# Optimization experiments

Hardware: AMD Instinct MI355X
Metric: run time of the kernel (lower is better)

The kernel has to match this reference:

```python
import jax, jax.numpy as jnp
import numpy as np
import math

CHUNK = 128  # hardcoded chunk_size in the original module


def setup_inputs() -> dict:
    key = jax.random.key(0)
    ks = jax.random.split(key, 6)
    B, C, T, H, W = 8, 256, 16, 8, 8
    KC, VC = 8192, 512  # key_channels, value_channels (dk = KC/heads = T*H*W = 1024)
    return {
        "x": jax.random.normal(ks[0], (B, C, T, H, W), dtype=jnp.float32),
        "Wk": jax.random.normal(ks[1], (KC, C), dtype=jnp.float32) * 0.02,
        "Wq": jax.random.normal(ks[2], (KC, C), dtype=jnp.float32) * 0.02,
        "Wv": jax.random.normal(ks[3], (VC, C), dtype=jnp.float32) * 0.02,
        "Wr": jax.random.normal(ks[4], (C, VC), dtype=jnp.float32) * 0.02,
        "br": jnp.zeros((C,), dtype=jnp.float32),
        "num_heads": 8,
    }


def reference(x, Wk, Wq, Wv, Wr, br, num_heads):
    B, C, T, H, W = x.shape
    N = T * H * W
    # 1x1x1 Conv3d == per-position linear projection
    k = jnp.einsum('oc,bcthw->bothw', Wk, x).reshape(B, num_heads, -1, N)
    q = jnp.einsum('oc,bcthw->bothw', Wq, x).reshape(B, num_heads, -1, N)
    v = jnp.einsum('oc,bcthw->bothw', Wv, x).reshape(B, num_heads, -1, N)
    dk = k.shape[2]  # == N by structural constraint of the original matmul
    # matmul(keys, q_chunk) over all chunks at once (matmul is linear in q):
    # contracts keys' position axis with queries' channel axis, as in torch.
    scores = jnp.matmul(k, q) / math.sqrt(dk)  # [B, h, dk, N]
    # softmax applied per query-chunk of size CHUNK along the last axis
    nchunks = N // CHUNK
    attn = jax.nn.softmax(
        scores.reshape(B, num_heads, dk, nchunks, CHUNK), axis=-1
    ).reshape(B, num_heads, dk, N)
    out = jnp.matmul(v, attn)  # [B, h, dv, N] (dk == N)
    out = out.reshape(B, -1, T, H, W)
    out = jnp.einsum('oc,bcthw->bothw', Wr, out) + br[None, :, None, None, None]
    return out
```

## Files before the change

kernel.cpp:

```cpp
#include <hip/hip_runtime.h>
#include <hip/hip_bf16.h>


using bf16x8 = __attribute__((ext_vector_type(8))) __bf16;
using f32x4  = __attribute__((ext_vector_type(4))) float;
using s16x4  = __attribute__((ext_vector_type(4))) short;

static __device__ __forceinline__ short f2b(float f) {
  union { float f; unsigned u; } v; v.f = f;
  unsigned r = v.u + 0x7fffu + ((v.u >> 16) & 1u);
  return (short)(r >> 16);
}

#define MFMA16(a, b, c) __builtin_amdgcn_mfma_f32_16x16x32_bf16((a), (b), (c), 0, 0, 0)

__global__ __launch_bounds__(256) void cvt_bf16(const float* __restrict__ in,
                                                short* __restrict__ out, int n) {
  int i = (blockIdx.x * 256 + threadIdx.x) * 4;
  if (i >= n) return;
  float4 v = *(const float4*)(in + i);
  s16x4 s = { f2b(v.x), f2b(v.y), f2b(v.z), f2b(v.w) };
  *(s16x4*)(out + i) = s;
}

__global__ __launch_bounds__(256) void tcvt(const float* __restrict__ in,
    short* __restrict__ outP, short* __restrict__ outT,
    int R, int C, long inB, long pB, long tB)
{
  __shared__ short tile[64][68];
  long bz = blockIdx.z;
  const float* src = in + bz * inB;
  int r0 = blockIdx.y * 64, c0 = blockIdx.x * 64;
  int t = threadIdx.x;
  int r = t >> 2, cq = (t & 3) * 16;
  #pragma unroll
  for (int e = 0; e < 16; e += 4) {
    float4 v = *(const float4*)(&src[(long)(r0 + r) * C + (c0 + cq + e)]);
    s16x4 s = { f2b(v.x), f2b(v.y), f2b(v.z), f2b(v.w) };
    *(s16x4*)(&tile[r][cq + e]) = s;
    if (outP) *(s16x4*)(&outP[bz * pB + (long)(r0 + r) * C + (c0 + cq + e)]) = s;
  }
  __syncthreads();
  int tr = t >> 2, re = (t & 3) * 16;
  short tmp[16];
  #pragma unroll
  for (int e = 0; e < 16; ++e) tmp[e] = tile[re + e][tr];
  short* dst = &outT[bz * tB + (long)(c0 + tr) * R + (r0 + re)];
  #pragma unroll
  for (int e = 0; e < 16; e += 4) *(s16x4*)(&dst[e]) = *(const s16x4*)(&tmp[e]);
}

template<bool F32OUT>
__global__ __launch_bounds__(256) void gemm_nt(
    const short* __restrict__ A, const short* __restrict__ B,
    void* __restrict__ C, const float* __restrict__ bias,
    int M, int N, int K, int lda, int ldb, int ldc,
    long aSB, long aSH, long bSB, long bSH, long cSB, long cSH, int nh)
{
  int batch = blockIdx.z;
  int hb = batch % nh, bb = batch / nh;
  const short* Ab = A + bb * aSB + hb * aSH;
  const short* Bb = B + bb * bSB + hb * bSH;
  long cOff = bb * cSB + hb * cSH;
  int m0 = blockIdx.y * 128, n0 = blockIdx.x * 128;
  __shared__ short As[128 * 72];
  __shared__ short Bs[128 * 72];
  int t = threadIdx.x;
  int lane = t & 63, wid = t >> 6;
  int wm = (wid >> 1) * 64, wn = (wid & 1) * 64;
  int rl = lane & 15, q = lane >> 4;
  f32x4 acc[4][4] = {};
  for (int k0 = 0; k0 < K; k0 += 64) {
    __syncthreads();
    #pragma unroll
    for (int it = 0; it < 4; ++it) {
      int e = (t + 256 * it) * 8;
      int row = e >> 6, col = e & 63;
      *(int4*)(&As[row * 72 + col]) = *(const int4*)(&Ab[(long)(m0 + row) * lda + (k0 + col)]);
      *(int4*)(&Bs[row * 72 + col]) = *(const int4*)(&Bb[(long)(n0 + row) * ldb + (k0 + col)]);
    }
    __syncthreads();
    #pragma unroll
    for (int kt = 0; kt < 2; ++kt) {
      int kq = kt * 32 + q * 8;
      bf16x8 af[4], bfv[4];
      #pragma unroll
      for (int mi = 0; mi < 4; ++mi) af[mi] = *(const bf16x8*)(&As[(wm + 16 * mi + rl) * 72 + kq]);
      #pragma unroll
      for (int ni = 0; ni < 4; ++ni) bfv[ni] = *(const bf16x8*)(&Bs[(wn + 16 * ni + rl) * 72 + kq]);
      #pragma unroll
      for (int mi = 0; mi < 4; ++mi)
        #pragma unroll
        for (int ni = 0; ni < 4; ++ni)
          acc[mi][ni] = MFMA16(af[mi], bfv[ni], acc[mi][ni]);
    }
  }
  #pragma unroll
  for (int mi = 0; mi < 4; ++mi)
    #pragma unroll
    for (int ni = 0; ni < 4; ++ni)
      #pragma unroll
      for (int r = 0; r < 4; ++r) {
        int row = m0 + wm + 16 * mi + 4 * q + r;
        int col = n0 + wn + 16 * ni + rl;
        float val = acc[mi][ni][r];
        if (F32OUT) {
          ((float*)C)[cOff + (long)row * ldc + col] = val + (bias ? bias[row] : 0.f);
        } else {
          ((short*)C)[cOff + (long)row * ldc + col] = f2b(val);
        }
      }
}

__global__ __launch_bounds__(256) void attn_fused(
    const short* __restrict__ Wk, const short* __restrict__ GT,
    const short* __restrict__ V, short* __restrict__ OT)
{
  __shared__ short smem[18432];
  short* As = smem;
  short* Bs = smem + 9216;
  short* aT = smem;
  int blk = blockIdx.x;
  int c = blk & 7, h = (blk >> 3) & 7, b = blk >> 6;
  int t = threadIdx.x, lane = t & 63, w = t >> 6;
  int rl = lane & 15, q = lane >> 4;
  const short* Wkh = Wk + (long)(h * 1024) * 256;
  const short* GTc = GT + ((long)(b * 8 + h) * 1024 + c * 128) * 256;
  const short* Vb  = V + (long)(b * 512 + h * 64) * 1024;
  f32x4 ot[2][4] = {};
  const float SC = 1.4426950408889634f / 32.0f;

  for (int ri = 0; ri < 8; ++ri) {
    f32x4 s[2][8] = {};
    for (int k0 = 0; k0 < 256; k0 += 64) {
      __syncthreads();
      #pragma unroll
      for (int it = 0; it < 4; ++it) {
        int e = (t + 256 * it) * 8;
        int row = e >> 6, col = e & 63;
        *(int4*)(&As[row * 72 + col]) = *(const int4*)(&Wkh[(long)(ri * 128 + row) * 256 + (k0 + col)]);
        *(int4*)(&Bs[row * 72 + col]) = *(const int4*)(&GTc[(long)row * 256 + (k0 + col)]);
      }
      __syncthreads();
      #pragma unroll
      for (int kt = 0; kt < 2; ++kt) {
        int kq = kt * 32 + q * 8;
        bf16x8 af[2], bfv[8];
        af[0] = *(const bf16x8*)(&As[(w * 32 + rl) * 72 + kq]);
        af[1] = *(const bf16x8*)(&As[(w * 32 + 16 + rl) * 72 + kq]);
        #pragma unroll
        for (int ni = 0; ni < 8; ++ni) bfv[ni] = *(const bf16x8*)(&Bs[(16 * ni + rl) * 72 + kq]);
        #pragma unroll
        for (int mi = 0; mi < 2; ++mi)
          #pragma unroll
          for (int ni = 0; ni < 8; ++ni)
            s[mi][ni] = MFMA16(af[mi], bfv[ni], s[mi][ni]);
      }
    }
    float mx[2][4], sm[2][4], rc[2][4];
    #pragma unroll
    for (int mi = 0; mi < 2; ++mi)
      #pragma unroll
      for (int r = 0; r < 4; ++r) {
        float m = s[mi][0][r];
        #pragma unroll
        for (int ni = 1; ni < 8; ++ni) m = fmaxf(m, s[mi][ni][r]);
        mx[mi][r] = m;
      }
    #pragma unroll
    for (int msk = 1; msk < 16; msk <<= 1)
      #pragma unroll
      for (int mi = 0; mi < 2; ++mi)
        #pragma unroll
        for (int r = 0; r < 4; ++r)
          mx[mi][r] = fmaxf(mx[mi][r], __shfl_xor(mx[mi][r], msk, 64));
    #pragma unroll
    for (int mi = 0; mi < 2; ++mi)
      #pragma unroll
      for (int r = 0; r < 4; ++r) sm[mi][r] = 0.f;
    #pragma unroll
    for (int mi = 0; mi < 2; ++mi)
      #pragma unroll
      for (int ni = 0; ni < 8; ++ni)
        #pragma unroll
        for (int r = 0; r < 4; ++r) {
          float p = exp2f((s[mi][ni][r] - mx[mi][r]) * SC);
          s[mi][ni][r] = p;
          sm[mi][r] += p;
        }
    #pragma unroll
    for (int msk = 1; msk < 16; msk <<= 1)
      #pragma unroll
      for (int mi = 0; mi < 2; ++mi)
        #pragma unroll
        for (int r = 0; r < 4; ++r)
          sm[mi][r] += __shfl_xor(sm[mi][r], msk, 64);
    #pragma unroll
    for (int mi = 0; mi < 2; ++mi)
      #pragma unroll
      for (int r = 0; r < 4; ++r) rc[mi][r] = __builtin_amdgcn_rcpf(sm[mi][r]);

    __syncthreads();
    #pragma unroll
    for (int mi = 0; mi < 2; ++mi)
      #pragma unroll
      for (int ni = 0; ni < 8; ++ni) {
        s16x4 pk = { f2b(s[mi][ni][0] * rc[mi][0]), f2b(s[mi][ni][1] * rc[mi][1]),
                     f2b(s[mi][ni][2] * rc[mi][2]), f2b(s[mi][ni][3] * rc[mi][3]) };
        int j  = 16 * ni + rl;
        int iL = 32 * w + 16 * mi + 4 * q;
        *(s16x4*)(&aT[j * 136 + iL]) = pk;
      }
    __syncthreads();
    #pragma unroll
    for (int kt = 0; kt < 4; ++kt) {
      int kq = kt * 32 + q * 8;
      bf16x8 pa[2], vb[4];
      pa[0] = *(const bf16x8*)(&aT[(32 * w + rl) * 136 + kq]);
      pa[1] = *(const bf16x8*)(&aT[(32 * w + 16 + rl) * 136 + kq]);
      #pragma unroll
      for (int nd = 0; nd < 4; ++nd)
        vb[nd] = *(const bf16x8*)(&Vb[(long)(16 * nd + rl) * 1024 + (ri * 128 + kq)]);
      #pragma unroll
      for (int mi = 0; mi < 2; ++mi)
        #pragma unroll
        for (int nd = 0; nd < 4; ++nd)
          ot[mi][nd] = MFMA16(pa[mi], vb[nd], ot[mi][nd]);
    }
  }
  short* OTb = OT + (long)(b * 1024 + c * 128) * 512 + h * 64;
  #pragma unroll
  for (int mi = 0; mi < 2; ++mi)
    #pragma unroll
    for (int nd = 0; nd < 4; ++nd)
      #pragma unroll
      for (int r = 0; r < 4; ++r) {
        int j = 32 * w + 16 * mi + 4 * q + r;
        int d = 16 * nd + rl;
        OTb[(long)j * 512 + d] = f2b(ot[mi][nd][r]);
      }
}

extern "C" void kernel_launch(void* const* d_in, const int* in_sizes, int n_in,
                              void* d_out, int out_size, void* d_ws, size_t ws_size,
                              hipStream_t stream)
{
  const float* x  = (const float*)d_in[0];
  const float* Wk = (const float*)d_in[1];
  const float* Wq = (const float*)d_in[2];
  const float* Wv = (const float*)d_in[3];
  const float* Wr = (const float*)d_in[4];
  const float* br = (const float*)d_in[5];
  float* out = (float*)d_out;

  char* ws = (char*)d_ws;
  short* Xbf = (short*)(ws + 0);
  short* XT  = (short*)(ws + 4194304);
  short* WqT = (short*)(ws + 8388608);
  short* Wkb = (short*)(ws + 12582912);
  short* Wvb = (short*)(ws + 16777216);
  short* Wrb = (short*)(ws + 17039360);
  short* Mb  = (short*)(ws + 17301504);
  short* GTb = (short*)(ws + 25690112);
  short* Vbf = (short*)(ws + 59244544);
  short* OTb = (short*)(ws + 67633152);

  tcvt<<<dim3(16, 4, 8), 256, 0, stream>>>(x, Xbf, XT, 256, 1024, 262144L, 262144L, 262144L);
  tcvt<<<dim3(4, 128, 1), 256, 0, stream>>>(Wq, nullptr, WqT, 8192, 256, 0L, 0L, 0L);
  cvt_bf16<<<2048, 256, 0, stream>>>(Wk, Wkb, 2097152);
  cvt_bf16<<<128, 256, 0, stream>>>(Wv, Wvb, 131072);
  cvt_bf16<<<128, 256, 0, stream>>>(Wr, Wrb, 131072);

  gemm_nt<false><<<dim3(2, 2, 64), 256, 0, stream>>>(Xbf, WqT, Mb, nullptr,
      256, 256, 1024, 1024, 8192, 256,
      262144L, 0L, 0L, 1024L, 524288L, 65536L, 8);
  gemm_nt<false><<<dim3(2, 8, 64), 256, 0, stream>>>(XT, Mb, GTb, nullptr,
      1024, 256, 256, 256, 256, 256,
      262144L, 0L, 524288L, 65536L, 2097152L, 262144L, 8);
  gemm_nt<false><<<dim3(8, 4, 8), 256, 0, stream>>>(Wvb, XT, Vbf, nullptr,
      512, 1024, 256, 256, 256, 1024,
      0L, 0L, 262144L, 0L, 524288L, 0L, 1);
  attn_fused<<<512, 256, 0, stream>>>(Wkb, GTb, Vbf, OTb);
  gemm_nt<true><<<dim3(8, 2, 8), 256, 0, stream>>>(Wrb, OTb, out, br,
      256, 1024, 512, 512, 512, 1024,
      0L, 0L, 524288L, 0L, 262144L, 0L, 1);
}
```

Baseline: 310.9 us.

## Use direct global-to-LDS loads with XOR swizzle and double-buffer Wk in attention

Replaces register-staged LDS fills in the projection GEMM and the fused attention kernel with global_load_lds 16-byte transfers into XOR-swizzled LDS tiles, removing the padding. The attention kernel now keeps the whole GT chunk resident in LDS and double-buffers the Wk tiles across 256-row groups, so each block does four larger score passes instead of eight. The P·V step is split into two halves through a swizzled transpose buffer. It uses 128KB of LDS with launch bounds of one block, which lowers occupancy and raises register pressure from the wider score accumulators.

New measurement: 291.4 us. -6.3%, faster.

```diff
diff --git a/kernel.cpp b/kernel.cpp
--- a/kernel.cpp
+++ b/kernel.cpp
@@ -10,6 +10,12 @@
   union { float f; unsigned u; } v; v.f = f;
   unsigned r = v.u + 0x7fffu + ((v.u >> 16) & 1u);
   return (short)(r >> 16);
+}
+
+static __device__ __forceinline__ void gll16(const void* g, void* l) {
+  __builtin_amdgcn_global_load_lds(
+      (const __attribute__((address_space(1))) void*)g,
+      (__attribute__((address_space(3))) void*)l, 16, 0, 0);
 }
 
 #define MFMA16(a, b, c) __builtin_amdgcn_mfma_f32_16x16x32_bf16((a), (b), (c), 0, 0, 0)
@@ -63,8 +69,8 @@
   const short* Bb = B + bb * bSB + hb * bSH;
   long cOff = bb * cSB + hb * cSH;
   int m0 = blockIdx.y * 128, n0 = blockIdx.x * 128;
-  __shared__ short As[128 * 72];
-  __shared__ short Bs[128 * 72];
+  __shared__ short As[128 * 64];
+  __shared__ short Bs[128 * 64];
   int t = threadIdx.x;
   int lane = t & 63, wid = t >> 6;
   int wm = (wid >> 1) * 64, wn = (wid & 1) * 64;
@@ -73,21 +79,28 @@
   for (int k0 = 0; k0 < K; k0 += 64) {
     __syncthreads();
     #pragma unroll
-    for (int it = 0; it < 4; ++it) {
-      int e = (t + 256 * it) * 8;
-      int row = e >> 6, col = e & 63;
-      *(int4*)(&As[row * 72 + col]) = *(const int4*)(&Ab[(long)(m0 + row) * lda + (k0 + col)]);
-      *(int4*)(&Bs[row * 72 + col]) = *(const int4*)(&Bb[(long)(n0 + row) * ldb + (k0 + col)]);
+    for (int j = 0; j < 4; ++j) {
+      int g = j * 256 + t;
+      int r = g >> 3, cc = g & 7;
+      int cs = cc ^ (r & 7);
+      gll16(&Ab[(long)(m0 + r) * lda + k0 + cs * 8], (char*)As + (j * 256 + wid * 64) * 16);
+      gll16(&Bb[(long)(n0 + r) * ldb + k0 + cs * 8], (char*)Bs + (j * 256 + wid * 64) * 16);
     }
     __syncthreads();
     #pragma unroll
     for (int kt = 0; kt < 2; ++kt) {
-      int kq = kt * 32 + q * 8;
+      int cq = kt * 4 + q;
       bf16x8 af[4], bfv[4];
       #pragma unroll
-      for (int mi = 0; mi < 4; ++mi) af[mi] = *(const bf16x8*)(&As[(wm + 16 * mi + rl) * 72 + kq]);
-      #pragma unroll
-      for (int ni = 0; ni < 4; ++ni) bfv[ni] = *(const bf16x8*)(&Bs[(wn + 16 * ni + rl) * 72 + kq]);
+      for (int mi = 0; mi < 4; ++mi) {
+        int R = wm + 16 * mi + rl;
+        af[mi] = *(const bf16x8*)((const char*)As + (R * 8 + (cq ^ (R & 7))) * 16);
+      }
+      #pragma unroll
+      for (int ni = 0; ni < 4; ++ni) {
+        int RN = wn + 16 * ni + rl;
+        bfv[ni] = *(const bf16x8*)((const char*)Bs + (RN * 8 + (cq ^ (RN & 7))) * 16);
+      }
       #pragma unroll
       for (int mi = 0; mi < 4; ++mi)
         #pragma unroll
@@ -112,14 +125,15 @@
       }
 }
 
-__global__ __launch_bounds__(256) void attn_fused(
+__global__ __launch_bounds__(256, 1) void attn_fused(
     const short* __restrict__ Wk, const short* __restrict__ GT,
     const short* __restrict__ V, short* __restrict__ OT)
 {
-  __shared__ short smem[18432];
-  short* As = smem;
-  short* Bs = smem + 9216;
-  short* aT = smem;
+  __shared__ short smem[65536];
+  short* Bs  = smem;
+  short* Ab0 = smem + 32768;
+  short* Ab1 = smem + 40960;
+  short* aT  = smem + 49152;
   int blk = blockIdx.x;
   int c = blk & 7, h = (blk >> 3) & 7, b = blk >> 6;
   int t = threadIdx.x, lane = t & 63, w = t >> 6;
@@ -130,36 +144,66 @@
   f32x4 ot[2][4] = {};
   const float SC = 1.4426950408889634f / 32.0f;
 
-  for (int ri = 0; ri < 8; ++ri) {
-    f32x4 s[2][8] = {};
-    for (int k0 = 0; k0 < 256; k0 += 64) {
+  #pragma unroll
+  for (int j = 0; j < 16; ++j) {
+    int g = j * 256 + t;
+    int r = g >> 5, cc = g & 31;
+    int cs = cc ^ (r & 7);
+    gll16(&GTc[(long)r * 256 + cs * 8], (char*)Bs + (j * 256 + w * 64) * 16);
+  }
+  {
+    #pragma unroll
+    for (int j = 0; j < 4; ++j) {
+      int g = j * 256 + t;
+      int r = g >> 2, cc = g & 3;
+      int cs = cc ^ ((r >> 1) & 3);
+      gll16(&Wkh[(long)r * 256 + cs * 8], (char*)Ab0 + (j * 256 + w * 64) * 16);
+    }
+  }
+  __syncthreads();
+
+  short* Acur = Ab0;
+  short* Anxt = Ab1;
+  for (int o = 0; o < 4; ++o) {
+    f32x4 s[4][8] = {};
+    for (int k0i = 0; k0i < 8; ++k0i) {
+      int k0 = k0i * 32;
+      int nRow = -1, nK = 0;
+      if (k0i < 7)      { nRow = o * 256;      nK = k0 + 32; }
+      else if (o < 3)   { nRow = (o + 1) * 256; nK = 0; }
+      if (nRow >= 0) {
+        #pragma unroll
+        for (int j = 0; j < 4; ++j) {
+          int g = j * 256 + t;
+          int r = g >> 2, cc = g & 3;
+          int cs = cc ^ ((r >> 1) & 3);
+          gll16(&Wkh[(long)(nRow + r) * 256 + nK + cs * 8],
+                (char*)Anxt + (j * 256 + w * 64) * 16);
+        }
+      }
+      bf16x8 af[4], bv[8];
+      #pragma unroll
+      for (int mi = 0; mi < 4; ++mi) {
+        int R = w * 64 + 16 * mi + rl;
+        af[mi] = *(const bf16x8*)((const char*)Acur + (R * 4 + (q ^ ((R >> 1) & 3))) * 16);
+      }
+      #pragma unroll
+      for (int ni = 0; ni < 8; ++ni) {
+        int Rj = 16 * ni + rl;
+        int cb = (k0 >> 3) + q;
+        bv[ni] = *(const bf16x8*)((const char*)Bs + (Rj * 32 + (cb ^ (Rj & 7))) * 16);
+      }
+      #pragma unroll
+      for (int mi = 0; mi < 4; ++mi)
+        #pragma unroll
+        for (int ni = 0; ni < 8; ++ni)
+          s[mi][ni] = MFMA16(af[mi], bv[ni], s[mi][ni]);
       __syncthreads();
-      #pragma unroll
-      for (int it = 0; it < 4; ++it) {
-        int e = (t + 256 * it) * 8;
-        int row = e >> 6, col = e & 63;
-        *(int4*)(&As[row * 72 + col]) = *(const int4*)(&Wkh[(long)(ri * 128 + row) * 256 + (k0 + col)]);
-        *(int4*)(&Bs[row * 72 + col]) = *(const int4*)(&GTc[(long)row * 256 + (k0 + col)]);
-      }
-      __syncthreads();
-      #pragma unroll
-      for (int kt = 0; kt < 2; ++kt) {
-        int kq = kt * 32 + q * 8;
-        bf16x8 af[2], bfv[8];
-        af[0] = *(const bf16x8*)(&As[(w * 32 + rl) * 72 + kq]);
-        af[1] = *(const bf16x8*)(&As[(w * 32 + 16 + rl) * 72 + kq]);
-        #pragma unroll
-        for (int ni = 0; ni < 8; ++ni) bfv[ni] = *(const bf16x8*)(&Bs[(16 * ni + rl) * 72 + kq]);
-        #pragma unroll
-        for (int mi = 0; mi < 2; ++mi)
-          #pragma unroll
-          for (int ni = 0; ni < 8; ++ni)
-            s[mi][ni] = MFMA16(af[mi], bfv[ni], s[mi][ni]);
-      }
-    }
-    float mx[2][4], sm[2][4], rc[2][4];
-    #pragma unroll
-    for (int mi = 0; mi < 2; ++mi)
+      short* tmp = Acur; Acur = Anxt; Anxt = tmp;
+    }
+    float mx[4][4], sm[4][4], rc[4][4];
+    #pragma unroll
+    for (int mi = 0; mi < 4; ++mi)
       #pragma unroll
       for (int r = 0; r < 4; ++r) {
         float m = s[mi][0][r];
@@ -170,16 +214,16 @@
     #pragma unroll
     for (int msk = 1; msk < 16; msk <<= 1)
       #pragma unroll
-      for (int mi = 0; mi < 2; ++mi)
+      for (int mi = 0; mi < 4; ++mi)
         #pragma unroll
         for (int r = 0; r < 4; ++r)
           mx[mi][r] = fmaxf(mx[mi][r], __shfl_xor(mx[mi][r], msk, 64));
     #pragma unroll
-    for (int mi = 0; mi < 2; ++mi)
+    for (int mi = 0; mi < 4; ++mi)
       #pragma unroll
       for (int r = 0; r < 4; ++r) sm[mi][r] = 0.f;
     #pragma unroll
-    for (int mi = 0; mi < 2; ++mi)
+    for (int mi = 0; mi < 4; ++mi)
       #pragma unroll
       for (int ni = 0; ni < 8; ++ni)
         #pragma unroll
@@ -191,41 +235,50 @@
     #pragma unroll
     for (int msk = 1; msk < 16; msk <<= 1)
       #pragma unroll
-      for (int mi = 0; mi < 2; ++mi)
+      for (int mi = 0; mi < 4; ++mi)
         #pragma unroll
         for (int r = 0; r < 4; ++r)
           sm[mi][r] += __shfl_xor(sm[mi][r], msk, 64);
     #pragma unroll
-    for (int mi = 0; mi < 2; ++mi)
+    for (int mi = 0; mi < 4; ++mi)
       #pragma unroll
       for (int r = 0; r < 4; ++r) rc[mi][r] = __builtin_amdgcn_rcpf(sm[mi][r]);
 
-    __syncthreads();
-    #pragma unroll
-    for (int mi = 0; mi < 2; ++mi)
-      #pragma unroll
-      for (int ni = 0; ni < 8; ++ni) {
-        s16x4 pk = { f2b(s[mi][ni][0] * rc[mi][0]), f2b(s[mi][ni][1] * rc[mi][1]),
-                     f2b(s[mi][ni][2] * rc[mi][2]), f2b(s[mi][ni][3] * rc[mi][3]) };
-        int j  = 16 * ni + rl;
-        int iL = 32 * w + 16 * mi + 4 * q;
-        *(s16x4*)(&aT[j * 136 + iL]) = pk;
-      }
-    __syncthreads();
-    #pragma unroll
-    for (int kt = 0; kt < 4; ++kt) {
-      int kq = kt * 32 + q * 8;
-      bf16x8 pa[2], vb[4];
-      pa[0] = *(const bf16x8*)(&aT[(32 * w + rl) * 136 + kq]);
-      pa[1] = *(const bf16x8*)(&aT[(32 * w + 16 + rl) * 136 + kq]);
-      #pragma unroll
-      for (int nd = 0; nd < 4; ++nd)
-        vb[nd] = *(const bf16x8*)(&Vb[(long)(16 * nd + rl) * 1024 + (ri * 128 + kq)]);
-      #pragma unroll
-      for (int mi = 0; mi < 2; ++mi)
+    #pragma unroll
+    for (int hf = 0; hf < 2; ++hf) {
+      if ((w >> 1) == hf) {
+        #pragma unroll
+        for (int mi = 0; mi < 4; ++mi)
+          #pragma unroll
+          for (int ni = 0; ni < 8; ++ni) {
+            s16x4 pk = { f2b(s[mi][ni][0] * rc[mi][0]), f2b(s[mi][ni][1] * rc[mi][1]),
+                         f2b(s[mi][ni][2] * rc[mi][2]), f2b(s[mi][ni][3] * rc[mi][3]) };
+            int j  = 16 * ni + rl;
+            int ci = (w & 1) * 8 + 2 * mi + (q >> 1);
+            *(s16x4*)((char*)aT + j * 256 + (ci ^ (j & 7)) * 16 + (q & 1) * 8) = pk;
+          }
+      }
+      __syncthreads();
+      #pragma unroll
+      for (int kt = 0; kt < 4; ++kt) {
+        bf16x8 pa[2], vv[4];
+        #pragma unroll
+        for (int mi = 0; mi < 2; ++mi) {
+          int Rj = 32 * w + 16 * mi + rl;
+          int ci = kt * 4 + q;
+          pa[mi] = *(const bf16x8*)((const char*)aT + Rj * 256 + (ci ^ (Rj & 7)) * 16);
+        }
+        int ig = o * 256 + hf * 128 + kt * 32 + q * 8;
         #pragma unroll
         for (int nd = 0; nd < 4; ++nd)
-          ot[mi][nd] = MFMA16(pa[mi], vb[nd], ot[mi][nd]);
+          vv[nd] = *(const bf16x8*)(&Vb[(long)(16 * nd + rl) * 1024 + ig]);
+        #pragma unroll
+        for (int mi = 0; mi < 2; ++mi)
+          #pragma unroll
+          for (int nd = 0; nd < 4; ++nd)
+            ot[mi][nd] = MFMA16(pa[mi], vv[nd], ot[mi][nd]);
+      }
+      __syncthreads();
     }
   }
   short* OTb = OT + (long)(b * 1024 + c * 128) * 512 + h * 64;
```
